# Kernel tuning notes

Hardware: AMD Instinct MI355X
Metric: run time of the kernel (lower is better)

Reference implementation:

```python
import jax, jax.numpy as jnp
import numpy as np

B, T, D = 64, 64, 256      # batch, decode steps, input_dim == wv_dim
TA = 128                   # encoder (attention) length
U = 256                    # units == att_dim
V = 50257                  # vocab_size


def hard_sigmoid(x):
    # keras hard_sigmoid
    return jnp.clip(0.2 * x + 0.5, 0.0, 1.0)


def setup_inputs() -> dict:
    key = jax.random.key(0)
    ks = jax.random.split(key, 8)
    n = lambda k, shape, sc: (jax.random.normal(k, shape, jnp.float32) * sc)
    return {
        "x": jax.random.normal(ks[0], (B, T, D), jnp.float32),
        "att": jax.random.normal(ks[1], (B, TA, U), jnp.float32),
        "kernel": n(ks[2], (D, 3 * U), 0.05),
        "recurrent_kernel": n(ks[3], (U, 3 * U), 0.05),
        "bias": jnp.zeros((3 * U,), jnp.float32),
        "after_att_kernel": n(ks[4], (U, 2 * U), 0.05),
        "after_att_bias": jnp.zeros((2 * U,), jnp.float32),
        "W_o1": n(ks[5], (U, V), 0.02),
        "embedding": n(ks[6], (V, D), 0.05),  # id2v table (non-trainable)
    }


def reference(x, att, kernel, recurrent_kernel, bias, after_att_kernel,
              after_att_bias, W_o1, embedding):
    u = recurrent_kernel.shape[0]
    # preprocess_input: time-distributed dense for all three gates at once
    xp = jnp.einsum('btd,dk->btk', x, kernel) + bias          # (B,T,3U)
    Kz, Kr, Kh = kernel[:, :u], kernel[:, u:2 * u], kernel[:, 2 * u:]
    Uz, Ur, Uh = (recurrent_kernel[:, :u], recurrent_kernel[:, u:2 * u],
                  recurrent_kernel[:, 2 * u:])
    Wa0, Wa1 = after_att_kernel[:, :u], after_att_kernel[:, u:2 * u]
    ba0, ba1 = after_att_bias[:u], after_att_bias[u:2 * u]

    h0 = jnp.zeros((x.shape[0], u), x.dtype)

    def step(h, xt):
        # attention over encoder outputs using previous hidden state
        e = jax.nn.softmax(jnp.einsum('btd,bd->bt', att, h))   # (B,TA)
        c = jnp.einsum('bt,btd->bd', e, att)                   # (B,U)
        # after-attention dense stack -> vocab distribution
        s = jnp.tanh(c @ Wa0 + ba0)
        s = jnp.tanh(s @ Wa1 + ba1)
        p = jax.nn.softmax(s @ W_o1)                           # (B,V)
        # embedding feedback (soft; hard_argmax=False)
        fb = p @ embedding                                     # (B,D)
        # GRU gates with feedback routed through the input kernel
        xz, xr, xh = xt[:, :u], xt[:, u:2 * u], xt[:, 2 * u:]
        z = hard_sigmoid(xz + fb @ Kz + h @ Uz)
        r = hard_sigmoid(xr + fb @ Kr + h @ Ur)
        hh = jnp.tanh(xh + fb @ Kh + (r * h) @ Uh)
        hn = z * h + (1.0 - z) * hh
        return hn, hn

    _, ys = jax.lax.scan(step, h0, jnp.swapaxes(xp, 0, 1))     # (T,B,U)
    return jnp.swapaxes(ys, 0, 1)                              # (B,T,U)
```

## Files before the change

kernel.cpp:

```cpp
#include <hip/hip_runtime.h>

#define BB 64
#define TT 64
#define DD 256
#define TAA 128
#define UU 256
#define VV 50257
#define NBLK 256
#define NV 208
#define NVK 224
#define W1ROWS 53248
#define EMBCOLS 53248
#define NT 512
#define OFF_W1   0
#define OFF_EMB  54912
#define OFF_P    114304
#define OFF_SA   129152
#define OFF_HL   146048
#define OFF_ZP   147072
#define SMEM_BYTES 147712

typedef __attribute__((ext_vector_type(4))) float floatx4;
typedef unsigned long long ull_t;

__device__ __forceinline__ float bf2f(unsigned short u) {
  union { unsigned int i; float f; } c; c.i = ((unsigned int)u) << 16; return c.f;
}
__device__ __forceinline__ unsigned short f2bf(float f) {
  union { float f; unsigned int i; } c; c.f = f;
  return (unsigned short)((c.i + 0x7fffu + ((c.i >> 16) & 1u)) >> 16);
}
__device__ __forceinline__ float hsig(float x) {
  return fminf(1.0f, fmaxf(0.0f, 0.2f * x + 0.5f));
}
__device__ __forceinline__ unsigned int pk4_fp8(float a, float b, float c, float d) {
  unsigned int r = 0;
  r = __builtin_amdgcn_cvt_pk_fp8_f32(a, b, r, false);
  r = __builtin_amdgcn_cvt_pk_fp8_f32(c, d, r, true);
  return r;
}

__device__ __forceinline__ void st_f(float* p, float v) {
  __hip_atomic_store(p, v, __ATOMIC_RELAXED, __HIP_MEMORY_SCOPE_AGENT);
}
__device__ __forceinline__ float ld_f(const float* p) {
  return __hip_atomic_load(p, __ATOMIC_RELAXED, __HIP_MEMORY_SCOPE_AGENT);
}
__device__ __forceinline__ void st_u16(unsigned short* p, unsigned short v) {
  __hip_atomic_store(p, v, __ATOMIC_RELAXED, __HIP_MEMORY_SCOPE_AGENT);
}
__device__ __forceinline__ void st_u32(unsigned int* p, unsigned int v) {
  __hip_atomic_store(p, v, __ATOMIC_RELAXED, __HIP_MEMORY_SCOPE_AGENT);
}
__device__ __forceinline__ unsigned int ld_u32(const unsigned int* p) {
  return __hip_atomic_load(p, __ATOMIC_RELAXED, __HIP_MEMORY_SCOPE_AGENT);
}
__device__ __forceinline__ ull_t ld_u64(const ull_t* p) {
  return __hip_atomic_load(p, __ATOMIC_RELAXED, __HIP_MEMORY_SCOPE_AGENT);
}

__device__ __forceinline__ void gbar(ull_t* bar, int phase) {
  asm volatile("s_waitcnt vmcnt(0)" ::: "memory");
  __syncthreads();
  if (threadIdx.x == 0) {
    ull_t* myc = (ull_t*)((char*)bar + 128 * (1 + (blockIdx.x & 7)));
    ull_t t1 = __hip_atomic_fetch_add(myc, 1ull, __ATOMIC_RELAXED,
                                      __HIP_MEMORY_SCOPE_AGENT) + 1ull;
    if (t1 == (ull_t)(32 * phase)) {
      __hip_atomic_fetch_add(bar, 1ull, __ATOMIC_RELAXED, __HIP_MEMORY_SCOPE_AGENT);
    }
    while (__hip_atomic_load(bar, __ATOMIC_RELAXED, __HIP_MEMORY_SCOPE_AGENT) <
           (ull_t)(8 * phase))
      __builtin_amdgcn_s_sleep(4);
  }
  __syncthreads();
}


__global__ void k_f2bf(const float* __restrict__ in, unsigned short* __restrict__ out, int n) {
  int i = blockIdx.x * 256 + threadIdx.x;
  int stride = gridDim.x * 256;
  for (; i < n; i += stride) out[i] = f2bf(in[i]);
}

__global__ void k_tw1(const float* __restrict__ w, unsigned int* __restrict__ o) {
  __shared__ float tile[32][33];
  const int bx = blockIdx.x, by = blockIdx.y;
  const int tx = threadIdx.x, ty = threadIdx.y;
#pragma unroll
  for (int i = 0; i < 4; ++i) {
    int k = by * 32 + ty + i * 8;
    int v = bx * 32 + tx;
    tile[ty + i * 8][tx] = (v < VV) ? w[(size_t)k * VV + v] : 0.0f;
  }
  __syncthreads();
  const int t = ty * 32 + tx;
  const int vl = t >> 3;
  const int cg = t & 7;
  unsigned int pk = pk4_fp8(tile[cg * 4 + 0][vl], tile[cg * 4 + 1][vl],
                            tile[cg * 4 + 2][vl], tile[cg * 4 + 3][vl]);
  o[(size_t)(bx * 32 + vl) * 64 + by * 8 + cg] = pk;
}

__global__ void k_temb(const float* __restrict__ e, unsigned int* __restrict__ o) {
  __shared__ float tile[32][33];
  const int bx = blockIdx.x, by = blockIdx.y;
  const int tx = threadIdx.x, ty = threadIdx.y;
#pragma unroll
  for (int i = 0; i < 4; ++i) {
    int v = bx * 32 + ty + i * 8;
    int d = by * 32 + tx;
    tile[ty + i * 8][tx] = (v < VV) ? e[(size_t)v * 256 + d] : 0.0f;
  }
  __syncthreads();
  const int t = ty * 32 + tx;
  const int dl = t >> 3;
  const int vg = t & 7;
  unsigned int pk = pk4_fp8(tile[vg * 4 + 0][dl], tile[vg * 4 + 1][dl],
                            tile[vg * 4 + 2][dl], tile[vg * 4 + 3][dl]);
  o[(size_t)(by * 32 + dl) * 13312 + bx * 8 + vg] = pk;
}

__global__ void k_xp(const float* __restrict__ x, const float* __restrict__ kern,
                     const float* __restrict__ bias, float* __restrict__ xp) {
  __shared__ float xs[256][20];
  const int r0 = blockIdx.x * 16;
  const int tid = threadIdx.x;
  for (int idx = tid; idx < 16 * 256; idx += 256) {
    int rr = idx >> 8;
    int k = idx & 255;
    xs[k][rr] = x[(size_t)(r0 + rr) * 256 + k];
  }
  __syncthreads();
  float acc[16][3];
#pragma unroll
  for (int rr = 0; rr < 16; ++rr) {
    acc[rr][0] = bias[tid];
    acc[rr][1] = bias[256 + tid];
    acc[rr][2] = bias[512 + tid];
  }
  for (int k = 0; k < 256; ++k) {
    float k0 = kern[k * 768 + tid];
    float k1 = kern[k * 768 + 256 + tid];
    float k2 = kern[k * 768 + 512 + tid];
#pragma unroll
    for (int rr = 0; rr < 16; ++rr) {
      float xv = xs[k][rr];
      acc[rr][0] = fmaf(xv, k0, acc[rr][0]);
      acc[rr][1] = fmaf(xv, k1, acc[rr][1]);
      acc[rr][2] = fmaf(xv, k2, acc[rr][2]);
    }
  }
  for (int rr = 0; rr < 16; ++rr) {
    xp[(size_t)(r0 + rr) * 768 + tid] = acc[rr][0];
    xp[(size_t)(r0 + rr) * 768 + 256 + tid] = acc[rr][1];
    xp[(size_t)(r0 + rr) * 768 + 512 + tid] = acc[rr][2];
  }
}


__global__ void __launch_bounds__(NT, 2) gru_main(
    const float* __restrict__ att,
    const float* __restrict__ aab,
    const unsigned short* __restrict__ kbf,
    const unsigned short* __restrict__ rkbf,
    const unsigned short* __restrict__ aabf,
    const float* __restrict__ xp,
    const unsigned int* __restrict__ w1g,
    const unsigned int* __restrict__ embg,
    unsigned int* __restrict__ s8,
    unsigned short* __restrict__ pfb,
    float* __restrict__ psum,
    float* __restrict__ fbp4,
    ull_t* __restrict__ hflag,
    ull_t* __restrict__ bar,
    float* __restrict__ y)
{
  extern __shared__ char smem[];
  char* w1p  = smem + OFF_W1;
  char* embp = smem + OFF_EMB;
  char* Pp   = smem + OFF_P;
  char* sAp  = smem + OFF_SA;
  float* red4  = (float*)(smem + OFF_SA);
  float* fbL   = (float*)(smem + OFF_SA + 8192);
  float* rhL   = (float*)(smem + OFF_SA + 9216);
  float* cL    = (float*)(smem + OFF_SA + 10240);
  float* s1L   = (float*)(smem + OFF_SA + 11264);
  float* s2L   = (float*)(smem + OFF_SA + 12288);
  float* eL    = (float*)(smem + OFF_SA + 13312);
  float* zredL = (float*)(smem + OFF_SA + 13824);
  float* hL    = (float*)(smem + OFF_HL);
  float* zpartL= (float*)(smem + OFF_ZP);

  const int blk = blockIdx.x;
  const int tid = threadIdx.x;
  const int b = blk;
  const int vbase = blk * NV;

  const int w = tid >> 6;
  const int lane = tid & 63;
  const int w2 = w & 3;
  const int half = w >> 2;
  const int lq = lane >> 4;
  const int li = lane & 15;
  const int hb = blk & 63;
  const int hq = blk >> 6;

  {
    unsigned int* dst = (unsigned int*)w1p;
    for (int i = tid; i < NV * 64; i += NT) {
      int r = i >> 6, c = i & 63;
      dst[r * 66 + c] = w1g[(size_t)(vbase + r) * 64 + c];
    }
    unsigned int* ed = (unsigned int*)embp;
    for (int i = tid; i < 256 * 52; i += NT) {
      int r = i / 52, c = i - r * 52;
      ed[r * 58 + c] = embg[(size_t)r * 13312 + blk * 52 + c];
    }
    for (int i = tid; i < 256 * 6; i += NT) {
      int r = i / 6, c = i - r * 6;
      ed[r * 58 + 52 + c] = 0u;
    }
    unsigned int* Pd = (unsigned int*)Pp;
    for (int i = tid; i < 64 * 6; i += NT) {
      int r = i / 6, c = i - r * 6;
      Pd[r * 58 + 52 + c] = 0u;
    }
  }

  auto attention = [&]() {
    {
      const int r = tid >> 2, q = tid & 3;
      const float* ar = att + (size_t)(b * TAA + r) * DD + q * 64;
      const float* hp = hL + q * 64;
      float l0 = 0.f, l1 = 0.f;
#pragma unroll
      for (int dd = 0; dd < 64; dd += 8) {
        float4 a0 = *reinterpret_cast<const float4*>(ar + dd);
        float4 a1 = *reinterpret_cast<const float4*>(ar + dd + 4);
        l0 += a0.x * hp[dd] + a0.y * hp[dd + 1] + a0.z * hp[dd + 2] + a0.w * hp[dd + 3];
        l1 += a1.x * hp[dd + 4] + a1.y * hp[dd + 5] + a1.z * hp[dd + 6] + a1.w * hp[dd + 7];
      }
      float s = l0 + l1;
      s += __shfl_xor(s, 1);
      s += __shfl_xor(s, 2);
      if (q == 0) eL[r] = s;
    }
    __syncthreads();
    if (tid < 64) {
      float l0 = eL[tid], l1 = eL[tid + 64];
      float m = fmaxf(l0, l1);
#pragma unroll
      for (int off = 32; off > 0; off >>= 1) m = fmaxf(m, __shfl_xor(m, off));
      float e0 = __expf(l0 - m), e1 = __expf(l1 - m);
      float s = e0 + e1;
#pragma unroll
      for (int off = 32; off > 0; off >>= 1) s += __shfl_xor(s, off);
      float inv = 1.0f / s;
      eL[tid] = e0 * inv;
      eL[tid + 64] = e1 * inv;
    }
    __syncthreads();
    {
      const int d = tid & 255, g = tid >> 8;
      const float* ab = att + (size_t)b * TAA * DD + d;
      float c0 = 0.f, c1 = 0.f;
#pragma unroll 4
      for (int ta = g * 64; ta < g * 64 + 64; ta += 2) {
        c0 += eL[ta] * ab[(size_t)ta * DD];
        c1 += eL[ta + 1] * ab[(size_t)(ta + 1) * DD];
      }
      red4[tid] = c0 + c1;
    }
    __syncthreads();
    if (tid < 256) cL[tid] = red4[tid] + red4[tid + 256];
    __syncthreads();
    {
      const int out = tid & 255, g = tid >> 8;
      float a0 = g ? 0.f : aab[out], a1 = 0.f;
      for (int k = g * 128; k < g * 128 + 128; k += 2) {
        a0 += cL[k] * bf2f(aabf[k * 512 + out]);
        a1 += cL[k + 1] * bf2f(aabf[(k + 1) * 512 + out]);
      }
      red4[tid] = a0 + a1;
    }
    __syncthreads();
    if (tid < 256) s1L[tid] = tanhf(red4[tid] + red4[tid + 256]);
    __syncthreads();
    {
      const int out = tid & 255, g = tid >> 8;
      float a0 = g ? 0.f : aab[256 + out], a1 = 0.f;
      for (int k = g * 128; k < g * 128 + 128; k += 2) {
        a0 += s1L[k] * bf2f(aabf[k * 512 + 256 + out]);
        a1 += s1L[k + 1] * bf2f(aabf[(k + 1) * 512 + 256 + out]);
      }
      red4[tid] = a0 + a1;
    }
    __syncthreads();
    if (tid < 256) s2L[tid] = tanhf(red4[tid] + red4[tid + 256]);
    __syncthreads();
    if (tid < 64) {
      unsigned int pk = pk4_fp8(s2L[4 * tid], s2L[4 * tid + 1],
                                s2L[4 * tid + 2], s2L[4 * tid + 3]);
      st_u32(s8 + b * 64 + tid, pk);
    }
  };

  auto helper_reduce = [&]() {
    {
      const int gl = tid >> 6;
      const int dq = tid & 63;
      float a0 = 0, a1 = 0, a2 = 0, a3 = 0;
      const ull_t* base = (const ull_t*)pfb + (size_t)hb * (256 * 64) + dq;
      const int g0 = hq * 64 + gl;
#pragma unroll
      for (int i = 0; i < 8; ++i) {
        ull_t u = ld_u64(base + (size_t)(g0 + i * 8) * 64);
        a0 += __uint_as_float((unsigned)(u << 16));
        a1 += __uint_as_float((unsigned)u & 0xffff0000u);
        a2 += __uint_as_float(((unsigned)(u >> 16)) & 0xffff0000u);
        a3 += __uint_as_float(((unsigned)(u >> 32)) & 0xffff0000u);
      }
      *reinterpret_cast<float4*>(red4 + gl * 256 + dq * 4) =
          make_float4(a0, a1, a2, a3);
    }
    __syncthreads();
    if (tid < 256) {
      float s = 0.f;
#pragma unroll
      for (int j = 0; j < 8; ++j) s += red4[tid + j * 256];
      st_f(fbp4 + ((size_t)hb * 4 + hq) * 256 + tid, s);
    }
    asm volatile("s_waitcnt vmcnt(0)" ::: "memory");
    __syncthreads();
    if (tid == 0)
      __hip_atomic_fetch_add(hflag + (size_t)hb * 16, 1ull, __ATOMIC_RELAXED,
                             __HIP_MEMORY_SCOPE_AGENT);
  };

  auto ca_step = [&](int t) {
    if (tid < 256) zredL[tid] = ld_f(psum + b * 256 + tid);
    __syncthreads();
    if (tid < 64) {
      float z2 = zredL[tid] + zredL[tid + 64] + zredL[tid + 128] + zredL[tid + 192];
#pragma unroll
      for (int off = 32; off > 0; off >>= 1) z2 += __shfl_xor(z2, off);
      if (tid == 0) zredL[0] = z2;
    }
    if (tid == 0) {
      while (__hip_atomic_load(hflag + (size_t)b * 16, __ATOMIC_RELAXED,
                               __HIP_MEMORY_SCOPE_AGENT) < (ull_t)(4 * (t + 1)))
        __builtin_amdgcn_s_sleep(2);
    }
    __syncthreads();
    if (tid < 256) {
      float invZ = 1.0f / zredL[0];
      const float* fp = fbp4 + (size_t)b * 1024;
      fbL[tid] = (ld_f(fp + tid) + ld_f(fp + 256 + tid) +
                  ld_f(fp + 512 + tid) + ld_f(fp + 768 + tid)) * invZ;
    }
    __syncthreads();
    const float* xprow = xp + (size_t)(b * 64 + t) * 768;
    float z0 = xprow[tid & 255], z1 = 0.f;
    const int out = tid & 255, g = tid >> 8;
    z0 = g ? 0.f : xprow[out];
    float r0 = g ? 0.f : xprow[256 + out], r1 = 0.f;
    for (int k = g * 128; k < g * 128 + 128; k += 2) {
      float fb0 = fbL[k], h0 = hL[k], fb1 = fbL[k + 1], h1 = hL[k + 1];
      const unsigned short* kp0 = kbf + k * 768 + out;
      const unsigned short* up0 = rkbf + k * 768 + out;
      z0 += fb0 * bf2f(kp0[0]) + h0 * bf2f(up0[0]);
      r0 += fb0 * bf2f(kp0[256]) + h0 * bf2f(up0[256]);
      z1 += fb1 * bf2f(kp0[768]) + h1 * bf2f(up0[768]);
      r1 += fb1 * bf2f(kp0[1024]) + h1 * bf2f(up0[1024]);
    }
    red4[tid] = z0 + z1;
    red4[512 + tid] = r0 + r1;
    __syncthreads();
    float zf = 0.f;
    if (tid < 256) {
      zf = red4[tid] + red4[tid + 256];
      float rf = red4[512 + tid] + red4[768 + tid];
      rhL[tid] = hsig(rf) * hL[tid];
    }
    __syncthreads();
    {
      float hp0 = g ? 0.f : xprow[512 + out], hp1 = 0.f;
      for (int k = g * 128; k < g * 128 + 128; k += 2) {
        hp0 += fbL[k] * bf2f(kbf[k * 768 + 512 + out]) +
               rhL[k] * bf2f(rkbf[k * 768 + 512 + out]);
        hp1 += fbL[k + 1] * bf2f(kbf[(k + 1) * 768 + 512 + out]) +
               rhL[k + 1] * bf2f(rkbf[(k + 1) * 768 + 512 + out]);
      }
      red4[1024 + tid] = hp0 + hp1;
    }
    __syncthreads();
    if (tid < 256) {
      float hh = tanhf(red4[1024 + tid] + red4[1280 + tid]);
      float z = hsig(zf);
      float hn = z * hL[tid] + (1.0f - z) * hh;
      y[(size_t)(b * 64 + t) * 256 + tid] = hn;
      hL[tid] = hn;
    }
    __syncthreads();
  };

  auto b_phase = [&]() {
    {
      unsigned int* sd = (unsigned int*)sAp;
      for (int i = tid; i < 4096; i += NT) {
        int r = i >> 6, c = i & 63;
        sd[r * 66 + c] = ld_u32(s8 + i);
      }
    }
    __syncthreads();
    long afr[8];
#pragma unroll
    for (int kk = 0; kk < 8; ++kk)
      afr[kk] = *reinterpret_cast<const long*>(sAp + (16 * w2 + li) * 264 + kk * 32 + lq * 8);
    float sacc[4] = {0.f, 0.f, 0.f, 0.f};
    const int vt0 = half ? 7 : 0;
    const int vt1 = half ? 13 : 7;
    for (int vt = vt0; vt < vt1; ++vt) {
      floatx4 lacc = (floatx4){0.f, 0.f, 0.f, 0.f};
#pragma unroll
      for (int kk = 0; kk < 8; ++kk) {
        long bfr = *reinterpret_cast<const long*>(w1p + (vt * 16 + li) * 264 + kk * 32 + lq * 8);
        lacc = __builtin_amdgcn_mfma_f32_16x16x32_fp8_fp8(afr[kk], bfr, lacc, 0, 0, 0);
      }
      const int v = vbase + vt * 16 + li;
      const bool ok = (v < VV);
#pragma unroll
      for (int q = 0; q < 4; ++q) {
        float p = ok ? __expf(lacc[q]) : 0.0f;
        sacc[q] += p;
        unsigned int pb = __builtin_amdgcn_cvt_pk_fp8_f32(p, 0.f, 0u, false);
        Pp[(16 * w2 + lq * 4 + q) * 232 + vt * 16 + li] = (char)(pb & 0xff);
      }
    }
#pragma unroll
    for (int q = 0; q < 4; ++q) {
      float s = sacc[q];
      s += __shfl_xor(s, 1);
      s += __shfl_xor(s, 2);
      s += __shfl_xor(s, 4);
      s += __shfl_xor(s, 8);
      if (li == 0) zpartL[(16 * w2 + lq * 4 + q) * 2 + half] = s;
    }
    __syncthreads();
    if (tid < 64) st_f(psum + tid * 256 + blk, zpartL[2 * tid] + zpartL[2 * tid + 1]);
    long pfr[7];
#pragma unroll
    for (int kk = 0; kk < 7; ++kk)
      pfr[kk] = *reinterpret_cast<const long*>(Pp + (16 * w2 + li) * 232 + kk * 32 + lq * 8);
    const int dt0 = half * 8;
#pragma unroll 4
    for (int dt = dt0; dt < dt0 + 8; ++dt) {
      floatx4 f = (floatx4){0.f, 0.f, 0.f, 0.f};
#pragma unroll
      for (int kk = 0; kk < 7; ++kk) {
        long efr = *reinterpret_cast<const long*>(embp + (dt * 16 + li) * 232 + kk * 32 + lq * 8);
        f = __builtin_amdgcn_mfma_f32_16x16x32_fp8_fp8(pfr[kk], efr, f, 0, 0, 0);
      }
#pragma unroll
      for (int q = 0; q < 4; ++q) {
        int row = 16 * w2 + lq * 4 + q;
        st_u16(pfb + ((size_t)(row * 256 + blk)) * 256 + dt * 16 + li, f2bf(f[q]));
      }
    }
  };

  __syncthreads();
  if (blk < BB) {
    if (tid < 256) hL[tid] = 0.0f;
    __syncthreads();
    attention();
  }
  gbar(bar, 1);
  for (int t = 0; t < TT; ++t) {
    b_phase();
    gbar(bar, 2 + 2 * t);
    helper_reduce();
    if (blk < BB) {
      ca_step(t);
      attention();
    }
    gbar(bar, 3 + 2 * t);
  }
}


extern "C" void kernel_launch(void* const* d_in, const int* in_sizes, int n_in,
                              void* d_out, int out_size, void* d_ws, size_t ws_size,
                              hipStream_t stream) {
  const float* x    = (const float*)d_in[0];
  const float* att  = (const float*)d_in[1];
  const float* kern = (const float*)d_in[2];
  const float* rk   = (const float*)d_in[3];
  const float* bias = (const float*)d_in[4];
  const float* aak  = (const float*)d_in[5];
  const float* aab  = (const float*)d_in[6];
  const float* w1   = (const float*)d_in[7];
  const float* emb  = (const float*)d_in[8];
  float* y = (float*)d_out;

  char* ws = (char*)d_ws;
  size_t o = 0;
  auto alloc = [&](size_t bytes) {
    char* p = ws + o;
    o += (bytes + 255) & ~(size_t)255;
    return p;
  };
  ull_t* bar   = (ull_t*)alloc(2048);
  ull_t* hflag = (ull_t*)alloc(8192);
  unsigned int* w1g  = (unsigned int*)alloc((size_t)W1ROWS * 256);
  unsigned int* embg = (unsigned int*)alloc((size_t)256 * EMBCOLS);
  unsigned short* kbf  = (unsigned short*)alloc((size_t)196608 * 2);
  unsigned short* rkbf = (unsigned short*)alloc((size_t)196608 * 2);
  unsigned short* aabf = (unsigned short*)alloc((size_t)131072 * 2);
  float* xp  = (float*)alloc((size_t)4096 * 768 * 4);
  unsigned int* s8 = (unsigned int*)alloc((size_t)64 * 64 * 4);
  unsigned short* pfb = (unsigned short*)alloc((size_t)64 * 256 * 256 * 2);
  float* psum = (float*)alloc((size_t)64 * 256 * 4);
  float* fbp4 = (float*)alloc((size_t)64 * 4 * 256 * 4);
  (void)ws_size; (void)in_sizes; (void)n_in; (void)out_size;

  static bool attr_done = false;
  if (!attr_done) {
    hipFuncSetAttribute((const void*)gru_main,
                        hipFuncAttributeMaxDynamicSharedMemorySize, SMEM_BYTES);
    attr_done = true;
  }

  hipMemsetAsync(bar, 0, 2048 + 8192, stream);
  hipLaunchKernelGGL(k_f2bf, dim3(768), dim3(256), 0, stream, kern, kbf, 196608);
  hipLaunchKernelGGL(k_f2bf, dim3(768), dim3(256), 0, stream, rk, rkbf, 196608);
  hipLaunchKernelGGL(k_f2bf, dim3(512), dim3(256), 0, stream, aak, aabf, 131072);
  hipLaunchKernelGGL(k_tw1, dim3(1664, 8), dim3(32, 8), 0, stream, w1, w1g);
  hipLaunchKernelGGL(k_temb, dim3(1664, 8), dim3(32, 8), 0, stream, emb, embg);
  hipLaunchKernelGGL(k_xp, dim3(256), dim3(256), 0, stream, x, kern, bias, xp);
  hipLaunchKernelGGL(gru_main, dim3(NBLK), dim3(NT), SMEM_BYTES, stream,
                     att, aab, kbf, rkbf, aabf, xp, w1g, embg, s8, pfb, psum,
                     fbp4, hflag, bar, y);
}
```

Before: 2.874 ms.

## Replace second grid barrier with counter wait and offload reductions to helper blocks

Drops the second grid-wide barrier of each step and uses an atomic counter that the 64 batch blocks bump after writing their fp8 attention state; every block spins on that counter before the next B phase. The feedback reduction tasks now run only on non-batch blocks (some take two tasks), so batch blocks go straight to the GRU step. The GRU and after-attention matvecs are restructured to 4-way k splits with paired bf16 loads, and the h·U part is hoisted before the feedback wait to overlap it. The risks are more spin-polling traffic, load imbalance between helper blocks, and memory-ordering subtleties with relaxed atomics.

```diff
diff --git a/kernel.cpp b/kernel.cpp
--- a/kernel.cpp
+++ b/kernel.cpp
@@ -203,8 +203,11 @@
   const int half = w >> 2;
   const int lq = lane >> 4;
   const int li = lane & 15;
-  const int hb = blk & 63;
-  const int hq = blk >> 6;
+  const int op = tid & 127;
+  const int g4 = tid >> 7;
+  const int k0 = g4 * 64;
+
+  ull_t* s8cnt = (ull_t*)((char*)bar + 1152);
 
   {
     unsigned int* dst = (unsigned int*)w1p;
@@ -276,28 +279,32 @@
     if (tid < 256) cL[tid] = red4[tid] + red4[tid + 256];
     __syncthreads();
     {
-      const int out = tid & 255, g = tid >> 8;
-      float a0 = g ? 0.f : aab[out], a1 = 0.f;
-      for (int k = g * 128; k < g * 128 + 128; k += 2) {
-        a0 += cL[k] * bf2f(aabf[k * 512 + out]);
-        a1 += cL[k + 1] * bf2f(aabf[(k + 1) * 512 + out]);
-      }
-      red4[tid] = a0 + a1;
-    }
-    __syncthreads();
-    if (tid < 256) s1L[tid] = tanhf(red4[tid] + red4[tid + 256]);
-    __syncthreads();
-    {
-      const int out = tid & 255, g = tid >> 8;
-      float a0 = g ? 0.f : aab[256 + out], a1 = 0.f;
-      for (int k = g * 128; k < g * 128 + 128; k += 2) {
-        a0 += s1L[k] * bf2f(aabf[k * 512 + 256 + out]);
-        a1 += s1L[k + 1] * bf2f(aabf[(k + 1) * 512 + 256 + out]);
-      }
-      red4[tid] = a0 + a1;
-    }
-    __syncthreads();
-    if (tid < 256) s2L[tid] = tanhf(red4[tid] + red4[tid + 256]);
+      float a0 = g4 ? 0.f : aab[2 * op], a1 = g4 ? 0.f : aab[2 * op + 1];
+      for (int k = k0; k < k0 + 64; ++k) {
+        float c = cL[k];
+        ushort2 w2a = *reinterpret_cast<const ushort2*>(aabf + k * 512 + 2 * op);
+        a0 += c * bf2f(w2a.x);
+        a1 += c * bf2f(w2a.y);
+      }
+      *reinterpret_cast<float2*>(red4 + g4 * 256 + 2 * op) = make_float2(a0, a1);
+    }
+    __syncthreads();
+    if (tid < 256)
+      s1L[tid] = tanhf(red4[tid] + red4[tid + 256] + red4[tid + 512] + red4[tid + 768]);
+    __syncthreads();
+    {
+      float a0 = g4 ? 0.f : aab[256 + 2 * op], a1 = g4 ? 0.f : aab[256 + 2 * op + 1];
+      for (int k = k0; k < k0 + 64; ++k) {
+        float c = s1L[k];
+        ushort2 w2a = *reinterpret_cast<const ushort2*>(aabf + k * 512 + 256 + 2 * op);
+        a0 += c * bf2f(w2a.x);
+        a1 += c * bf2f(w2a.y);
+      }
+      *reinterpret_cast<float2*>(red4 + g4 * 256 + 2 * op) = make_float2(a0, a1);
+    }
+    __syncthreads();
+    if (tid < 256)
+      s2L[tid] = tanhf(red4[tid] + red4[tid + 256] + red4[tid + 512] + red4[tid + 768]);
     __syncthreads();
     if (tid < 64) {
       unsigned int pk = pk4_fp8(s2L[4 * tid], s2L[4 * tid + 1],
@@ -306,13 +313,14 @@
     }
   };
 
-  auto helper_reduce = [&]() {
+  auto do_task = [&](int task) {
+    const int thb = task & 63, thq = task >> 6;
     {
       const int gl = tid >> 6;
       const int dq = tid & 63;
       float a0 = 0, a1 = 0, a2 = 0, a3 = 0;
-      const ull_t* base = (const ull_t*)pfb + (size_t)hb * (256 * 64) + dq;
-      const int g0 = hq * 64 + gl;
+      const ull_t* base = (const ull_t*)pfb + (size_t)thb * (256 * 64) + dq;
+      const int g0 = thq * 64 + gl;
 #pragma unroll
       for (int i = 0; i < 8; ++i) {
         ull_t u = ld_u64(base + (size_t)(g0 + i * 8) * 64);
@@ -329,17 +337,30 @@
       float s = 0.f;
 #pragma unroll
       for (int j = 0; j < 8; ++j) s += red4[tid + j * 256];
-      st_f(fbp4 + ((size_t)hb * 4 + hq) * 256 + tid, s);
+      st_f(fbp4 + ((size_t)thb * 4 + thq) * 256 + tid, s);
     }
     asm volatile("s_waitcnt vmcnt(0)" ::: "memory");
     __syncthreads();
     if (tid == 0)
-      __hip_atomic_fetch_add(hflag + (size_t)hb * 16, 1ull, __ATOMIC_RELAXED,
+      __hip_atomic_fetch_add(hflag + (size_t)thb * 16, 1ull, __ATOMIC_RELAXED,
                              __HIP_MEMORY_SCOPE_AGENT);
+    __syncthreads();
   };
 
   auto ca_step = [&](int t) {
+    const float* xprow = xp + (size_t)(b * 64 + t) * 768;
     if (tid < 256) zredL[tid] = ld_f(psum + b * 256 + tid);
+    float zA = g4 ? 0.f : xprow[2 * op];
+    float zB = g4 ? 0.f : xprow[2 * op + 1];
+    float rA = g4 ? 0.f : xprow[256 + 2 * op];
+    float rB = g4 ? 0.f : xprow[256 + 2 * op + 1];
+    for (int k = k0; k < k0 + 64; ++k) {
+      float h = hL[k];
+      ushort2 uz = *reinterpret_cast<const ushort2*>(rkbf + k * 768 + 2 * op);
+      ushort2 ur = *reinterpret_cast<const ushort2*>(rkbf + k * 768 + 256 + 2 * op);
+      zA += h * bf2f(uz.x); zB += h * bf2f(uz.y);
+      rA += h * bf2f(ur.x); rB += h * bf2f(ur.y);
+    }
     __syncthreads();
     if (tid < 64) {
       float z2 = zredL[tid] + zredL[tid + 64] + zredL[tid + 128] + zredL[tid + 192];
@@ -360,43 +381,42 @@
                   ld_f(fp + 512 + tid) + ld_f(fp + 768 + tid)) * invZ;
     }
     __syncthreads();
-    const float* xprow = xp + (size_t)(b * 64 + t) * 768;
-    float z0 = xprow[tid & 255], z1 = 0.f;
-    const int out = tid & 255, g = tid >> 8;
-    z0 = g ? 0.f : xprow[out];
-    float r0 = g ? 0.f : xprow[256 + out], r1 = 0.f;
-    for (int k = g * 128; k < g * 128 + 128; k += 2) {
-      float fb0 = fbL[k], h0 = hL[k], fb1 = fbL[k + 1], h1 = hL[k + 1];
-      const unsigned short* kp0 = kbf + k * 768 + out;
-      const unsigned short* up0 = rkbf + k * 768 + out;
-      z0 += fb0 * bf2f(kp0[0]) + h0 * bf2f(up0[0]);
-      r0 += fb0 * bf2f(kp0[256]) + h0 * bf2f(up0[256]);
-      z1 += fb1 * bf2f(kp0[768]) + h1 * bf2f(up0[768]);
-      r1 += fb1 * bf2f(kp0[1024]) + h1 * bf2f(up0[1024]);
-    }
-    red4[tid] = z0 + z1;
-    red4[512 + tid] = r0 + r1;
+    for (int k = k0; k < k0 + 64; ++k) {
+      float fb = fbL[k];
+      ushort2 kz = *reinterpret_cast<const ushort2*>(kbf + k * 768 + 2 * op);
+      ushort2 kr = *reinterpret_cast<const ushort2*>(kbf + k * 768 + 256 + 2 * op);
+      zA += fb * bf2f(kz.x); zB += fb * bf2f(kz.y);
+      rA += fb * bf2f(kr.x); rB += fb * bf2f(kr.y);
+    }
+    *reinterpret_cast<float2*>(red4 + g4 * 256 + 2 * op) = make_float2(zA, zB);
+    *reinterpret_cast<float2*>(red4 + 1024 + g4 * 256 + 2 * op) = make_float2(rA, rB);
     __syncthreads();
     float zf = 0.f;
     if (tid < 256) {
-      zf = red4[tid] + red4[tid + 256];
-      float rf = red4[512 + tid] + red4[768 + tid];
+      float rf = 0.f;
+#pragma unroll
+      for (int j = 0; j < 4; ++j) {
+        zf += red4[j * 256 + tid];
+        rf += red4[1024 + j * 256 + tid];
+      }
       rhL[tid] = hsig(rf) * hL[tid];
     }
     __syncthreads();
     {
-      float hp0 = g ? 0.f : xprow[512 + out], hp1 = 0.f;
-      for (int k = g * 128; k < g * 128 + 128; k += 2) {
-        hp0 += fbL[k] * bf2f(kbf[k * 768 + 512 + out]) +
-               rhL[k] * bf2f(rkbf[k * 768 + 512 + out]);
-        hp1 += fbL[k + 1] * bf2f(kbf[(k + 1) * 768 + 512 + out]) +
-               rhL[k + 1] * bf2f(rkbf[(k + 1) * 768 + 512 + out]);
-      }
-      red4[1024 + tid] = hp0 + hp1;
+      float hA = g4 ? 0.f : xprow[512 + 2 * op];
+      float hB = g4 ? 0.f : xprow[512 + 2 * op + 1];
+      for (int k = k0; k < k0 + 64; ++k) {
+        float fb = fbL[k], rh = rhL[k];
+        ushort2 kh = *reinterpret_cast<const ushort2*>(kbf + k * 768 + 512 + 2 * op);
+        ushort2 uh = *reinterpret_cast<const ushort2*>(rkbf + k * 768 + 512 + 2 * op);
+        hA += fb * bf2f(kh.x) + rh * bf2f(uh.x);
+        hB += fb * bf2f(kh.y) + rh * bf2f(uh.y);
+      }
+      *reinterpret_cast<float2*>(red4 + g4 * 256 + 2 * op) = make_float2(hA, hB);
     }
     __syncthreads();
     if (tid < 256) {
-      float hh = tanhf(red4[1024 + tid] + red4[1280 + tid]);
+      float hh = tanhf(red4[tid] + red4[tid + 256] + red4[tid + 512] + red4[tid + 768]);
       float z = hsig(zf);
       float hn = z * hL[tid] + (1.0f - z) * hh;
       y[(size_t)(b * 64 + t) * 256 + tid] = hn;
@@ -475,17 +495,36 @@
     if (tid < 256) hL[tid] = 0.0f;
     __syncthreads();
     attention();
+    asm volatile("s_waitcnt vmcnt(0)" ::: "memory");
+    __syncthreads();
+    if (tid == 0)
+      __hip_atomic_fetch_add(s8cnt, 1ull, __ATOMIC_RELAXED, __HIP_MEMORY_SCOPE_AGENT);
   }
   gbar(bar, 1);
   for (int t = 0; t < TT; ++t) {
     b_phase();
-    gbar(bar, 2 + 2 * t);
-    helper_reduce();
-    if (blk < BB) {
+    gbar(bar, 2 + t);
+    if (blk >= BB) {
+      do_task(blk - 64);
+      if (blk >= 192) do_task(blk);
+    } else {
       ca_step(t);
-      attention();
-    }
-    gbar(bar, 3 + 2 * t);
+      if (t + 1 < TT) {
+        attention();
+        asm volatile("s_waitcnt vmcnt(0)" ::: "memory");
+        __syncthreads();
+        if (tid == 0)
+          __hip_atomic_fetch_add(s8cnt, 1ull, __ATOMIC_RELAXED, __HIP_MEMORY_SCOPE_AGENT);
+      }
+    }
+    if (t + 1 < TT) {
+      if (tid == 0) {
+        while (__hip_atomic_load(s8cnt, __ATOMIC_RELAXED, __HIP_MEMORY_SCOPE_AGENT) <
+               (ull_t)(64 * (t + 2)))
+          __builtin_amdgcn_s_sleep(2);
+      }
+      __syncthreads();
+    }
   }
 }
 
```

After: 9.980 ms. +247.3%, slower.
